# Kernel optimization log

Hardware: AMD Instinct MI355X
Metric: run time of the kernel (lower is better)

## Reference

```python
import jax, jax.numpy as jnp
import numpy as np

B, HW, FEAT = 64, 196, 2048
EMB, HID, ATT, VOCAB, T = 512, 1024, 512, 10000, 20
STEPS = T - 1  # pack_padded_sequence uses lengths - 1


def setup_inputs() -> dict:
    key = jax.random.key(0)
    ks = jax.random.split(key, 16)
    rn = lambda k, s, sc=0.02: jax.random.normal(k, s, jnp.float32) * sc
    return {
        "features": jax.random.normal(ks[0], (B, HW, FEAT), jnp.float32),
        "captions": jax.random.randint(ks[1], (B, T), 0, VOCAB),
        "lengths": jnp.full((B,), T, jnp.int32),  # uniform lengths -> constant batch per step
        "E": rn(ks[2], (VOCAB, EMB)),
        "W_feat": rn(ks[3], (EMB, FEAT)), "b_feat": jnp.zeros((EMB,), jnp.float32),
        "W1": rn(ks[4], (ATT, EMB)), "b1": jnp.zeros((ATT,), jnp.float32),
        "W2": rn(ks[5], (ATT, HID)), "b2": jnp.zeros((ATT,), jnp.float32),
        "V": rn(ks[6], (1, ATT)), "bV": jnp.zeros((1,), jnp.float32),
        "W_hi": rn(ks[7], (HID, EMB)), "b_hi": jnp.zeros((HID,), jnp.float32),
        "W_ci": rn(ks[8], (HID, EMB)), "b_ci": jnp.zeros((HID,), jnp.float32),
        "W_ih": rn(ks[9], (4 * HID, 2 * EMB)), "b_ih": jnp.zeros((4 * HID,), jnp.float32),
        "W_hh": rn(ks[10], (4 * HID, HID)), "b_hh": jnp.zeros((4 * HID,), jnp.float32),
        "W_out": rn(ks[11], (VOCAB, HID)), "b_out": jnp.zeros((VOCAB,), jnp.float32),
    }


def reference(features, captions, lengths, E, W_feat, b_feat, W1, b1, W2, b2,
              V, bV, W_hi, b_hi, W_ci, b_ci, W_ih, b_ih, W_hh, b_hh, W_out, b_out):
    # features -> embed space: [B, HW, EMB]
    f = jnp.einsum('bhc,ec->bhe', features, W_feat) + b_feat
    fmean = f.mean(axis=1)                      # [B, EMB]
    hx0 = fmean @ W_hi.T + b_hi                 # [B, HID]
    cx0 = fmean @ W_ci.T + b_ci                 # [B, HID]
    fa = jnp.einsum('bhe,ae->bha', f, W1) + b1  # W1(features), [B, HW, ATT]

    emb = E[captions]                           # [B, T, EMB]
    xs = jnp.swapaxes(emb[:, :STEPS], 0, 1)     # [STEPS, B, EMB] teacher-forced inputs

    def step(carry, x):
        hx, cx = carry
        # Bahdanau attention
        ha = hx @ W2.T + b2                             # [B, ATT]
        score = jnp.tanh(fa + ha[:, None, :])           # [B, HW, ATT]
        logits = jnp.einsum('bha,oa->bho', score, V) + bV   # [B, HW, 1]
        w = jax.nn.softmax(logits, axis=1)              # softmax over HW
        ctx = jnp.sum(w * f, axis=1)                    # [B, EMB]
        # LSTMCell (PyTorch gate order: i, f, g, o)
        inp = jnp.concatenate([x, ctx], axis=1)         # [B, 2*EMB]
        gates = inp @ W_ih.T + b_ih + hx @ W_hh.T + b_hh
        i_g, f_g, g_g, o_g = jnp.split(gates, 4, axis=1)
        cx_n = jax.nn.sigmoid(f_g) * cx + jax.nn.sigmoid(i_g) * jnp.tanh(g_g)
        hx_n = jax.nn.sigmoid(o_g) * jnp.tanh(cx_n)
        out = hx_n @ W_out.T + b_out                    # dropout = identity (eval)
        return (hx_n, cx_n), out

    _, outs = jax.lax.scan(step, (hx0, cx0), xs)        # [STEPS, B, VOCAB]
    # torch.cat(outputs) over constant per-step batch == flatten time-major
    return outs.reshape(STEPS * B, VOCAB)
```

## Files before the change

kernel.cpp:

```cpp
#include <hip/hip_runtime.h>
#include <hip/hip_bf16.h>
#include <math.h>

#define BB 64
#define HW 196
#define FEAT 2048
#define EMB 512
#define HID 1024
#define ATT 512
#define VOCAB 10000
#define TT 20
#define STEPS 19

using bfrag = __attribute__((ext_vector_type(8))) short;
using f32x4 = __attribute__((ext_vector_type(4))) float;

__device__ __forceinline__ float sigmoid_fast(float x) { return 1.0f / (1.0f + __expf(-x)); }
__device__ __forceinline__ float tanh_fast(float x) {
    float e = __expf(2.0f * x);
    return 1.0f - 2.0f / (e + 1.0f);
}
__device__ __forceinline__ ushort f2bf_rne(float f) {
    unsigned u = __float_as_uint(f);
    unsigned r = (u + 0x7FFFu + ((u >> 16) & 1u)) >> 16;
    return (ushort)r;
}
__device__ __forceinline__ float bf2f(ushort h) {
    return __uint_as_float(((unsigned)h) << 16);
}
__device__ __forceinline__ int sw_idx(int row, int g) { return row * 4 + (g ^ ((row >> 1) & 3)); }

__global__ __launch_bounds__(256) void k_split(const float* __restrict__ x,
                                               ushort* __restrict__ hi,
                                               ushort* __restrict__ lo, int n)
{
    int i4 = (blockIdx.x * 256 + threadIdx.x) * 4;
    if (i4 >= n) return;
    float4 v = *(const float4*)(x + i4);
    float av[4] = {v.x, v.y, v.z, v.w};
    #pragma unroll
    for (int j = 0; j < 4; ++j) {
        ushort h = f2bf_rne(av[j]);
        hi[i4 + j] = h;
        lo[i4 + j] = f2bf_rne(av[j] - bf2f(h));
    }
}

template<bool NFAST>
__global__ __launch_bounds__(256) void mfma_g(
    const float* __restrict__ A,
    const ushort* __restrict__ Bhi, const ushort* __restrict__ Blo,
    const float* __restrict__ bias, float* __restrict__ C,
    int N, int K, int Bld, int ldc, int NXB, int NMB)
{
    __shared__ __align__(16) ushort sAh[256 * 8];
    __shared__ __align__(16) ushort sAl[256 * 8];
    __shared__ __align__(16) ushort sBh[512 * 8];
    __shared__ __align__(16) ushort sBl[512 * 8];

    const int tid = threadIdx.x;

    const int nwg = NXB * NMB;
    const int q = nwg >> 3, r = nwg & 7;
    const int xcd = blockIdx.x & 7, sidx = blockIdx.x >> 3;
    const int wg = (xcd < r) ? (xcd * (q + 1) + sidx)
                             : (r * (q + 1) + (xcd - r) * q + sidx);
    int im, inb;
    if (NFAST) { inb = wg % NXB; im = wg / NXB; }
    else       { im = wg % NMB; inb = wg / NMB; }
    const int m0 = im * 64;
    const int n0 = inb * 128;

    const int lane = tid & 63;
    const int w = tid >> 6;
    const int mh = (w & 1) * 32;
    const int nh = (w >> 1) * 64;
    const int g = lane >> 4, l15 = lane & 15;

    f32x4 acc[2][4] = {};

    for (int k0 = 0; k0 < K; k0 += 32) {
        __syncthreads();
        {
            int r_ = tid >> 2, g_ = tid & 3;
            const float* ap = A + (size_t)(m0 + r_) * K + k0 + g_ * 8;
            float av[8];
            *(float4*)(av)     = *(const float4*)(ap);
            *(float4*)(av + 4) = *(const float4*)(ap + 4);
            bfrag vh, vl;
            #pragma unroll
            for (int j = 0; j < 8; ++j) {
                ushort h = f2bf_rne(av[j]);
                vh[j] = (short)h;
                vl[j] = (short)f2bf_rne(av[j] - bf2f(h));
            }
            int c = sw_idx(r_, g_) * 8;
            *(bfrag*)&sAh[c] = vh;
            *(bfrag*)&sAl[c] = vl;
        }
        #pragma unroll
        for (int i = 0; i < 4; ++i) {
            int c = tid + i * 256;
            int pl = c >> 9, idx2 = c & 511;
            int r_ = idx2 >> 2, g_ = idx2 & 3;
            int brow = min(n0 + r_, N - 1);
            const ushort* src = (pl ? Blo : Bhi) + (size_t)brow * Bld + k0 + g_ * 8;
            int cc = sw_idx(r_, g_) * 8;
            if (pl) *(bfrag*)&sBl[cc] = *(const bfrag*)src;
            else    *(bfrag*)&sBh[cc] = *(const bfrag*)src;
        }
        __syncthreads();

        bfrag ah[2], al[2], bh[4], bl[4];
        #pragma unroll
        for (int s = 0; s < 2; ++s) {
            int c = sw_idx(mh + s * 16 + l15, g) * 8;
            ah[s] = *(const bfrag*)&sAh[c];
            al[s] = *(const bfrag*)&sAl[c];
        }
        #pragma unroll
        for (int u = 0; u < 4; ++u) {
            int c = sw_idx(nh + u * 16 + l15, g) * 8;
            bh[u] = *(const bfrag*)&sBh[c];
            bl[u] = *(const bfrag*)&sBl[c];
        }
        #pragma unroll
        for (int s = 0; s < 2; ++s)
            #pragma unroll
            for (int u = 0; u < 4; ++u) {
                acc[s][u] = __builtin_amdgcn_mfma_f32_16x16x32_bf16(ah[s], bh[u], acc[s][u], 0, 0, 0);
                acc[s][u] = __builtin_amdgcn_mfma_f32_16x16x32_bf16(ah[s], bl[u], acc[s][u], 0, 0, 0);
                acc[s][u] = __builtin_amdgcn_mfma_f32_16x16x32_bf16(al[s], bh[u], acc[s][u], 0, 0, 0);
            }
    }

    #pragma unroll
    for (int s = 0; s < 2; ++s)
        #pragma unroll
        for (int u = 0; u < 4; ++u) {
            int col = n0 + nh + u * 16 + l15;
            if (col < N) {
                float bv = bias ? bias[col] : 0.f;
                #pragma unroll
                for (int rr = 0; rr < 4; ++rr) {
                    int row = m0 + mh + s * 16 + g * 4 + rr;
                    C[(size_t)row * ldc + col] = acc[s][u][rr] + bv;
                }
            }
        }
}

__global__ __launch_bounds__(256) void k_fmean2(const float* __restrict__ f,
                                                float* __restrict__ fmean)
{
    __shared__ float part[128];
    int blk = blockIdx.x;
    int b = blk >> 2, eq = blk & 3;
    int el = threadIdx.x & 127, half = threadIdx.x >> 7;
    int e = eq * 128 + el;
    const float* fb = f + (size_t)b * HW * EMB + e;
    float s = 0.f;
    int h0 = half * 98;
    for (int h = h0; h < h0 + 98; ++h) s += fb[(size_t)h * EMB];
    if (half) part[el] = s;
    __syncthreads();
    if (!half) fmean[b * EMB + e] = (s + part[el]) * (1.0f / HW);
}

__global__ __launch_bounds__(256) void k_init2(
    const float* __restrict__ fmean,
    const float* __restrict__ W_hi, const float* __restrict__ b_hi,
    const float* __restrict__ W_ci, const float* __restrict__ b_ci,
    float* __restrict__ hx, float* __restrict__ cx,
    ushort* __restrict__ hxp_h, ushort* __restrict__ hxp_l)
{
    int o = blockIdx.x * 256 + threadIdx.x;
    int b = o >> 11, uu = o & 2047;
    bool isC = uu >= 1024;
    int u = uu & 1023;
    const float4* wr = (const float4*)((isC ? W_ci : W_hi) + (size_t)u * EMB);
    const float4* fm = (const float4*)(fmean + (size_t)b * EMB);
    float s = isC ? b_ci[u] : b_hi[u];
    #pragma unroll 8
    for (int k = 0; k < EMB / 4; ++k) {
        float4 wv = wr[k], xv = fm[k];
        s += wv.x*xv.x + wv.y*xv.y + wv.z*xv.z + wv.w*xv.w;
    }
    int idx = b * HID + u;
    if (isC) cx[idx] = s;
    else {
        hx[idx] = s;
        ushort hh = f2bf_rne(s);
        hxp_h[idx] = hh;
        hxp_l[idx] = f2bf_rne(s - bf2f(hh));
    }
}

__global__ __launch_bounds__(128) void k_embed(const int* __restrict__ cap,
                                               const float* __restrict__ E,
                                               float* __restrict__ xs_f)
{
    int blk = blockIdx.x;
    int t = blk / BB, b = blk % BB;
    int c = cap[b * TT + t];
    const float4* src = (const float4*)(E + (size_t)c * EMB);
    float4* dst = (float4*)(xs_f + ((size_t)t * BB + b) * EMB);
    dst[threadIdx.x] = src[threadIdx.x];
}

__global__ __launch_bounds__(256) void k_ha(
    const float* __restrict__ hx, const float* __restrict__ W2,
    const float* __restrict__ b2, float* __restrict__ ha)
{
    __shared__ __align__(16) float hx_s[8][1028];
    __shared__ float part[256];
    const int tid = threadIdx.x;
    const int a0 = (blockIdx.x >> 3) * 16;
    const int b0 = (blockIdx.x & 7) * 8;

    for (int i = tid; i < 8 * 256; i += 256) {
        int r = i >> 8, c4 = i & 255;
        *(float4*)&hx_s[r][c4 * 4] = *(const float4*)(hx + (size_t)(b0 + r) * HID + c4 * 4);
    }
    __syncthreads();

    const int a_i = tid >> 4;
    const int b_i = (tid >> 1) & 7;
    const int half = tid & 1;
    const float4* wr = (const float4*)(W2 + (size_t)(a0 + a_i) * HID + half * 512);
    const float* xr = &hx_s[b_i][half * 512];
    float s = 0.f;
    #pragma unroll 8
    for (int i = 0; i < 128; ++i) {
        float4 w = wr[i];
        float4 x = *(const float4*)(xr + i * 4);
        s += w.x*x.x + w.y*x.y + w.z*x.z + w.w*x.w;
    }
    part[tid] = s;
    __syncthreads();
    if (!half)
        ha[(size_t)(b0 + b_i) * ATT + a0 + a_i] = part[tid] + part[tid + 1] + b2[a0 + a_i];
}

__global__ __launch_bounds__(1024) void k_att(
    const float* __restrict__ f, const float* __restrict__ fa,
    const float* __restrict__ ha, const float* __restrict__ V,
    ushort* __restrict__ ctx_hi, ushort* __restrict__ ctx_lo)
{
    __shared__ __align__(16) float smem[2048];
    const int b = blockIdx.x;
    const int tid = threadIdx.x;
    const int lane = tid & 63;
    const int wid = tid >> 6;

    float* ha_s = smem;
    float* V_s  = smem + 512;
    float* w_s  = smem + 1024;
    float* red  = smem + 1280;
    float* pc   = smem + 1536;

    if (tid < ATT) { ha_s[tid] = ha[b * ATT + tid]; V_s[tid] = V[tid]; }
    __syncthreads();

    for (int h = wid; h < HW; h += 16) {
        const float4* fr = (const float4*)(fa + ((size_t)b * HW + h) * ATT);
        float s = 0.f;
        #pragma unroll
        for (int q = 0; q < 2; ++q) {
            int i4 = q * 64 + lane;
            float4 fv = fr[i4];
            float4 hv = *(const float4*)&ha_s[i4 * 4];
            float4 vv = *(const float4*)&V_s[i4 * 4];
            s += tanh_fast(fv.x + hv.x) * vv.x + tanh_fast(fv.y + hv.y) * vv.y
               + tanh_fast(fv.z + hv.z) * vv.z + tanh_fast(fv.w + hv.w) * vv.w;
        }
        #pragma unroll
        for (int off = 32; off > 0; off >>= 1) s += __shfl_down(s, off);
        if (lane == 0) w_s[h] = s;
    }
    __syncthreads();

    float v = (tid < HW) ? w_s[tid] : -INFINITY;
    if (tid < 256) red[tid] = v;
    __syncthreads();
    for (int s2 = 128; s2 > 0; s2 >>= 1) {
        if (tid < s2) red[tid] = fmaxf(red[tid], red[tid + s2]);
        __syncthreads();
    }
    float mx = red[0];
    __syncthreads();
    float e = (tid < HW) ? __expf(v - mx) : 0.f;
    if (tid < 256) red[tid] = e;
    __syncthreads();
    for (int s2 = 128; s2 > 0; s2 >>= 1) {
        if (tid < s2) red[tid] += red[tid + s2];
        __syncthreads();
    }
    float inv = 1.0f / red[0];
    if (tid < HW) w_s[tid] = e * inv;
    __syncthreads();

    {
        int e0 = tid & 511, grp = tid >> 9;
        const float* fb = f + (size_t)b * HW * EMB + e0;
        float s = 0.f;
        int h0 = grp * 98;
        for (int h = h0; h < h0 + 98; ++h)
            s = fmaf(w_s[h], fb[(size_t)h * EMB], s);
        if (grp) pc[e0] = s;
        __syncthreads();
        if (!grp) {
            float c = s + pc[e0];
            ushort ch = f2bf_rne(c);
            ctx_hi[b * EMB + e0] = ch;
            ctx_lo[b * EMB + e0] = f2bf_rne(c - bf2f(ch));
        }
    }
}

__global__ __launch_bounds__(512) void k_gates_lstm(
    const float* __restrict__ gxs_t,
    const ushort* __restrict__ cth, const ushort* __restrict__ ctl,
    const ushort* __restrict__ hxh, const ushort* __restrict__ hxl,
    const ushort* __restrict__ wihh, const ushort* __restrict__ wihl,
    const ushort* __restrict__ whhh, const ushort* __restrict__ whhl,
    const float* __restrict__ b_ih, const float* __restrict__ b_hh,
    float* __restrict__ hx, float* __restrict__ cx,
    ushort* __restrict__ nxh, ushort* __restrict__ nxl,
    float* __restrict__ hx_all_t)
{
    __shared__ float sg[2][64][16];
    const int tid = threadIdx.x, bk = blockIdx.x;
    const int lane = tid & 63, wid = tid >> 6;
    const int mt = wid & 3, kh = wid >> 2;
    const int l15 = lane & 15, g = lane >> 4;
    const int arow = mt * 16 + l15;
    const int ncol = (l15 >> 2) * 1024 + bk * 4 + (l15 & 3);
    const int koff = g * 8;

    f32x4 acc0 = {}, acc1 = {};

    if (kh == 0) {
        {
            const ushort* ah = cth + (size_t)arow * 512 + koff;
            const ushort* al = ctl + (size_t)arow * 512 + koff;
            const ushort* bh = wihh + (size_t)ncol * 1024 + 512 + koff;
            const ushort* bl = wihl + (size_t)ncol * 1024 + 512 + koff;
            #pragma unroll 4
            for (int kk = 0; kk < 16; ++kk) {
                bfrag a_h = *(const bfrag*)(ah + kk * 32);
                bfrag a_l = *(const bfrag*)(al + kk * 32);
                bfrag b_h = *(const bfrag*)(bh + kk * 32);
                bfrag b_l = *(const bfrag*)(bl + kk * 32);
                acc0 = __builtin_amdgcn_mfma_f32_16x16x32_bf16(a_h, b_h, acc0, 0, 0, 0);
                acc1 = __builtin_amdgcn_mfma_f32_16x16x32_bf16(a_h, b_l, acc1, 0, 0, 0);
                acc1 = __builtin_amdgcn_mfma_f32_16x16x32_bf16(a_l, b_h, acc1, 0, 0, 0);
            }
        }
        {
            const ushort* ah = hxh + (size_t)arow * 1024 + koff;
            const ushort* al = hxl + (size_t)arow * 1024 + koff;
            const ushort* bh = whhh + (size_t)ncol * 1024 + koff;
            const ushort* bl = whhl + (size_t)ncol * 1024 + koff;
            #pragma unroll 4
            for (int kk = 0; kk < 8; ++kk) {
                bfrag a_h = *(const bfrag*)(ah + kk * 32);
                bfrag a_l = *(const bfrag*)(al + kk * 32);
                bfrag b_h = *(const bfrag*)(bh + kk * 32);
                bfrag b_l = *(const bfrag*)(bl + kk * 32);
                acc0 = __builtin_amdgcn_mfma_f32_16x16x32_bf16(a_h, b_h, acc0, 0, 0, 0);
                acc1 = __builtin_amdgcn_mfma_f32_16x16x32_bf16(a_h, b_l, acc1, 0, 0, 0);
                acc1 = __builtin_amdgcn_mfma_f32_16x16x32_bf16(a_l, b_h, acc1, 0, 0, 0);
            }
        }
    } else {
        const ushort* ah = hxh + (size_t)arow * 1024 + 256 + koff;
        const ushort* al = hxl + (size_t)arow * 1024 + 256 + koff;
        const ushort* bh = whhh + (size_t)ncol * 1024 + 256 + koff;
        const ushort* bl = whhl + (size_t)ncol * 1024 + 256 + koff;
        #pragma unroll 4
        for (int kk = 0; kk < 24; ++kk) {
            bfrag a_h = *(const bfrag*)(ah + kk * 32);
            bfrag a_l = *(const bfrag*)(al + kk * 32);
            bfrag b_h = *(const bfrag*)(bh + kk * 32);
            bfrag b_l = *(const bfrag*)(bl + kk * 32);
            acc0 = __builtin_amdgcn_mfma_f32_16x16x32_bf16(a_h, b_h, acc0, 0, 0, 0);
            acc1 = __builtin_amdgcn_mfma_f32_16x16x32_bf16(a_h, b_l, acc1, 0, 0, 0);
            acc1 = __builtin_amdgcn_mfma_f32_16x16x32_bf16(a_l, b_h, acc1, 0, 0, 0);
        }
    }

    #pragma unroll
    for (int rr = 0; rr < 4; ++rr)
        sg[kh][mt * 16 + g * 4 + rr][l15] = acc0[rr] + acc1[rr];
    __syncthreads();

    if (tid < 256) {
        int b = tid >> 2, uu = tid & 3;
        int u = bk * 4 + uu;
        const float* gx = gxs_t + (size_t)b * 4096;
        float gi = sg[0][b][uu]      + sg[1][b][uu]      + gx[u]        + b_ih[u]        + b_hh[u];
        float gf = sg[0][b][4 + uu]  + sg[1][b][4 + uu]  + gx[1024 + u] + b_ih[1024 + u] + b_hh[1024 + u];
        float gg = sg[0][b][8 + uu]  + sg[1][b][8 + uu]  + gx[2048 + u] + b_ih[2048 + u] + b_hh[2048 + u];
        float go = sg[0][b][12 + uu] + sg[1][b][12 + uu] + gx[3072 + u] + b_ih[3072 + u] + b_hh[3072 + u];
        int idx = b * 1024 + u;
        float c = sigmoid_fast(gf) * cx[idx] + sigmoid_fast(gi) * tanh_fast(gg);
        float h = sigmoid_fast(go) * tanh_fast(c);
        cx[idx] = c;
        hx[idx] = h;
        hx_all_t[idx] = h;
        ushort hh = f2bf_rne(h);
        nxh[idx] = hh;
        nxl[idx] = f2bf_rne(h - bf2f(hh));
    }
}

extern "C" void kernel_launch(void* const* d_in, const int* in_sizes, int n_in,
                              void* d_out, int out_size, void* d_ws, size_t ws_size,
                              hipStream_t stream) {
    const float* features = (const float*)d_in[0];
    const int*   captions = (const int*)d_in[1];
    const float* E      = (const float*)d_in[3];
    const float* W_feat = (const float*)d_in[4];
    const float* b_feat = (const float*)d_in[5];
    const float* W1     = (const float*)d_in[6];
    const float* b1     = (const float*)d_in[7];
    const float* W2     = (const float*)d_in[8];
    const float* b2     = (const float*)d_in[9];
    const float* V      = (const float*)d_in[10];
    const float* W_hi   = (const float*)d_in[12];
    const float* b_hi   = (const float*)d_in[13];
    const float* W_ci   = (const float*)d_in[14];
    const float* b_ci   = (const float*)d_in[15];
    const float* W_ih   = (const float*)d_in[16];
    const float* b_ih   = (const float*)d_in[17];
    const float* W_hh   = (const float*)d_in[18];
    const float* b_hh   = (const float*)d_in[19];
    const float* W_out  = (const float*)d_in[20];
    const float* b_out  = (const float*)d_in[21];
    float* out = (float*)d_out;

    float* ws = (float*)d_ws;
    float* f_buf   = ws;
    float* fa_buf  = f_buf + 6422528;
    float* fmean   = fa_buf + 6422528;
    float* hx      = fmean + 32768;
    float* cx      = hx + 65536;
    float* hx_all  = cx + 65536;
    float* ha      = hx_all + 1310720;
    float* xs_f    = ha + 32768;
    float* gxs     = xs_f + 622592;
    ushort* p = (ushort*)(gxs + 4980736);
    ushort* wfeat_hi = p;            p += 1048576;
    ushort* wfeat_lo = p;            p += 1048576;
    ushort* w1_hi    = p;            p += 262144;
    ushort* w1_lo    = p;            p += 262144;
    ushort* wih_hi   = p;            p += 4194304;
    ushort* wih_lo   = p;            p += 4194304;
    ushort* whh_hi   = p;            p += 4194304;
    ushort* whh_lo   = p;            p += 4194304;
    ushort* ctx_hi   = p;            p += 32768;
    ushort* ctx_lo   = p;            p += 32768;
    ushort* hxp      = p;            p += 262144;
    ushort* wout_hi = (ushort*)f_buf;
    ushort* wout_lo = wout_hi + 10240000;

    k_split<<<1048576 / 4 / 256, 256, 0, stream>>>(W_feat, wfeat_hi, wfeat_lo, 1048576);
    k_split<<<262144 / 4 / 256, 256, 0, stream>>>(W1, w1_hi, w1_lo, 262144);
    k_split<<<4194304 / 4 / 256, 256, 0, stream>>>(W_ih, wih_hi, wih_lo, 4194304);
    k_split<<<4194304 / 4 / 256, 256, 0, stream>>>(W_hh, whh_hi, whh_lo, 4194304);
    k_embed<<<STEPS * BB, 128, 0, stream>>>(captions, E, xs_f);
    mfma_g<true><<<784, 256, 0, stream>>>(
        features, wfeat_hi, wfeat_lo, b_feat, f_buf, 512, 2048, 2048, 512, 4, 196);
    mfma_g<true><<<784, 256, 0, stream>>>(
        f_buf, w1_hi, w1_lo, b1, fa_buf, 512, 512, 512, 512, 4, 196);
    mfma_g<false><<<608, 256, 0, stream>>>(
        xs_f, wih_hi, wih_lo, nullptr, gxs, 4096, 512, 1024, 4096, 32, 19);
    k_fmean2<<<256, 256, 0, stream>>>(f_buf, fmean);
    k_init2<<<512, 256, 0, stream>>>(fmean, W_hi, b_hi, W_ci, b_ci,
                                     hx, cx, hxp, hxp + 65536);

    for (int t = 0; t < STEPS; ++t) {
        ushort* hx_rd = hxp + (size_t)(t & 1) * 131072;
        ushort* hx_wr = hxp + (size_t)((t + 1) & 1) * 131072;
        k_ha<<<256, 256, 0, stream>>>(hx, W2, b2, ha);
        k_att<<<BB, 1024, 0, stream>>>(f_buf, fa_buf, ha, V, ctx_hi, ctx_lo);
        k_gates_lstm<<<256, 512, 0, stream>>>(
            gxs + (size_t)t * BB * 4096,
            ctx_hi, ctx_lo, hx_rd, hx_rd + 65536,
            wih_hi, wih_lo, whh_hi, whh_lo, b_ih, b_hh,
            hx, cx, hx_wr, hx_wr + 65536,
            hx_all + (size_t)t * BB * HID);
    }

    k_split<<<10240000 / 4 / 256, 256, 0, stream>>>(W_out, wout_hi, wout_lo, 10240000);
    mfma_g<false><<<1501, 256, 0, stream>>>(
        hx_all, wout_hi, wout_lo, b_out, out, VOCAB, HID, 1024, VOCAB, 79, 19);
}
```

Measured before the change: 1.573 ms.

## Store attention projection in bf16 and use direct global-to-LDS loads for B

The W1 projection output (fa) is now written as bf16 instead of fp32, which halves the bytes the per-step attention kernel reads from it on each of the 19 steps. The attention kernel keeps ha and V in registers instead of shared memory. The GEMM's B-tile staging now uses global_load_lds direct-to-LDS loads with addresses precomputed outside the k-loop. The workspace layout is reshuffled to make room for the bf16 buffer. Rounding fa to bf16 adds precision loss inside the tanh attention scores.

Result: slower. 1.983 ms (+26.1%).

```diff
diff --git a/kernel.cpp b/kernel.cpp
--- a/kernel.cpp
+++ b/kernel.cpp
@@ -46,11 +46,12 @@
     }
 }
 
-template<bool NFAST>
+template<bool NFAST, bool BF16OUT>
 __global__ __launch_bounds__(256) void mfma_g(
     const float* __restrict__ A,
     const ushort* __restrict__ Bhi, const ushort* __restrict__ Blo,
     const float* __restrict__ bias, float* __restrict__ C,
+    ushort* __restrict__ C16,
     int N, int K, int Bld, int ldc, int NXB, int NMB)
 {
     __shared__ __align__(16) ushort sAh[256 * 8];
@@ -77,16 +78,33 @@
     const int nh = (w >> 1) * 64;
     const int g = lane >> 4, l15 = lane & 15;
 
+    const int rA = tid >> 2, gA = tid & 3;
+    const float* apA = A + (size_t)(m0 + rA) * K + gA * 8;
+    const int cA = sw_idx(rA, gA) * 8;
+
+    const ushort* bsrc[4];
+    ushort* bdst[4];
+    #pragma unroll
+    for (int i = 0; i < 4; ++i) {
+        int cbase = i * 256 + w * 64;
+        int plane = cbase >> 9;
+        int ccb = cbase & 511;
+        int cc = ccb + lane;
+        int row = cc >> 2;
+        int g_ = (cc & 3) ^ ((row >> 1) & 3);
+        int brow = min(n0 + row, N - 1);
+        bsrc[i] = (plane ? Blo : Bhi) + (size_t)brow * Bld + g_ * 8;
+        bdst[i] = (plane ? sBl : sBh) + ccb * 8;
+    }
+
     f32x4 acc[2][4] = {};
 
     for (int k0 = 0; k0 < K; k0 += 32) {
         __syncthreads();
         {
-            int r_ = tid >> 2, g_ = tid & 3;
-            const float* ap = A + (size_t)(m0 + r_) * K + k0 + g_ * 8;
             float av[8];
-            *(float4*)(av)     = *(const float4*)(ap);
-            *(float4*)(av + 4) = *(const float4*)(ap + 4);
+            *(float4*)(av)     = *(const float4*)(apA + k0);
+            *(float4*)(av + 4) = *(const float4*)(apA + k0 + 4);
             bfrag vh, vl;
             #pragma unroll
             for (int j = 0; j < 8; ++j) {
@@ -94,21 +112,14 @@
                 vh[j] = (short)h;
                 vl[j] = (short)f2bf_rne(av[j] - bf2f(h));
             }
-            int c = sw_idx(r_, g_) * 8;
-            *(bfrag*)&sAh[c] = vh;
-            *(bfrag*)&sAl[c] = vl;
-        }
-        #pragma unroll
-        for (int i = 0; i < 4; ++i) {
-            int c = tid + i * 256;
-            int pl = c >> 9, idx2 = c & 511;
-            int r_ = idx2 >> 2, g_ = idx2 & 3;
-            int brow = min(n0 + r_, N - 1);
-            const ushort* src = (pl ? Blo : Bhi) + (size_t)brow * Bld + k0 + g_ * 8;
-            int cc = sw_idx(r_, g_) * 8;
-            if (pl) *(bfrag*)&sBl[cc] = *(const bfrag*)src;
-            else    *(bfrag*)&sBh[cc] = *(const bfrag*)src;
-        }
+            *(bfrag*)&sAh[cA] = vh;
+            *(bfrag*)&sAl[cA] = vl;
+        }
+        #pragma unroll
+        for (int i = 0; i < 4; ++i)
+            __builtin_amdgcn_global_load_lds(
+                (const __attribute__((address_space(1))) void*)(bsrc[i] + k0),
+                (__attribute__((address_space(3))) void*)bdst[i], 16, 0, 0);
         __syncthreads();
 
         bfrag ah[2], al[2], bh[4], bl[4];
@@ -144,7 +155,9 @@
                 #pragma unroll
                 for (int rr = 0; rr < 4; ++rr) {
                     int row = m0 + mh + s * 16 + g * 4 + rr;
-                    C[(size_t)row * ldc + col] = acc[s][u][rr] + bv;
+                    float v = acc[s][u][rr] + bv;
+                    if (BF16OUT) C16[(size_t)row * ldc + col] = f2bf_rne(v);
+                    else         C[(size_t)row * ldc + col] = v;
                 }
             }
         }
@@ -243,37 +256,34 @@
 }
 
 __global__ __launch_bounds__(1024) void k_att(
-    const float* __restrict__ f, const float* __restrict__ fa,
+    const float* __restrict__ f, const ushort* __restrict__ fa16,
     const float* __restrict__ ha, const float* __restrict__ V,
     ushort* __restrict__ ctx_hi, ushort* __restrict__ ctx_lo)
 {
-    __shared__ __align__(16) float smem[2048];
+    __shared__ __align__(16) float smem[1024];
     const int b = blockIdx.x;
     const int tid = threadIdx.x;
     const int lane = tid & 63;
     const int wid = tid >> 6;
 
-    float* ha_s = smem;
-    float* V_s  = smem + 512;
-    float* w_s  = smem + 1024;
-    float* red  = smem + 1280;
-    float* pc   = smem + 1536;
-
-    if (tid < ATT) { ha_s[tid] = ha[b * ATT + tid]; V_s[tid] = V[tid]; }
-    __syncthreads();
+    float* w_s = smem;
+    float* red = smem + 256;
+    float* pc  = smem + 512;
+
+    float hr[8], vr[8];
+    {
+        const float4* hp = (const float4*)(ha + (size_t)b * ATT + lane * 8);
+        const float4* vp = (const float4*)(V + lane * 8);
+        *(float4*)(hr) = hp[0]; *(float4*)(hr + 4) = hp[1];
+        *(float4*)(vr) = vp[0]; *(float4*)(vr + 4) = vp[1];
+    }
 
     for (int h = wid; h < HW; h += 16) {
-        const float4* fr = (const float4*)(fa + ((size_t)b * HW + h) * ATT);
+        bfrag fv = *(const bfrag*)(fa16 + ((size_t)b * HW + h) * ATT + lane * 8);
         float s = 0.f;
         #pragma unroll
-        for (int q = 0; q < 2; ++q) {
-            int i4 = q * 64 + lane;
-            float4 fv = fr[i4];
-            float4 hv = *(const float4*)&ha_s[i4 * 4];
-            float4 vv = *(const float4*)&V_s[i4 * 4];
-            s += tanh_fast(fv.x + hv.x) * vv.x + tanh_fast(fv.y + hv.y) * vv.y
-               + tanh_fast(fv.z + hv.z) * vv.z + tanh_fast(fv.w + hv.w) * vv.w;
-        }
+        for (int j = 0; j < 8; ++j)
+            s += tanh_fast(bf2f((ushort)fv[j]) + hr[j]) * vr[j];
         #pragma unroll
         for (int off = 32; off > 0; off >>= 1) s += __shfl_down(s, off);
         if (lane == 0) w_s[h] = s;
@@ -442,15 +452,14 @@
 
     float* ws = (float*)d_ws;
     float* f_buf   = ws;
-    float* fa_buf  = f_buf + 6422528;
-    float* fmean   = fa_buf + 6422528;
+    float* gxs     = f_buf + 6422528;
+    float* xs_f    = gxs + 4980736;
+    float* fmean   = xs_f + 622592;
     float* hx      = fmean + 32768;
     float* cx      = hx + 65536;
     float* hx_all  = cx + 65536;
     float* ha      = hx_all + 1310720;
-    float* xs_f    = ha + 32768;
-    float* gxs     = xs_f + 622592;
-    ushort* p = (ushort*)(gxs + 4980736);
+    ushort* p = (ushort*)(ha + 32768);
     ushort* wfeat_hi = p;            p += 1048576;
     ushort* wfeat_lo = p;            p += 1048576;
     ushort* w1_hi    = p;            p += 262144;
@@ -462,6 +471,7 @@
     ushort* ctx_hi   = p;            p += 32768;
     ushort* ctx_lo   = p;            p += 32768;
     ushort* hxp      = p;            p += 262144;
+    ushort* fa16     = p;            p += 6422528;
     ushort* wout_hi = (ushort*)f_buf;
     ushort* wout_lo = wout_hi + 10240000;
 
@@ -470,12 +480,15 @@
     k_split<<<4194304 / 4 / 256, 256, 0, stream>>>(W_ih, wih_hi, wih_lo, 4194304);
     k_split<<<4194304 / 4 / 256, 256, 0, stream>>>(W_hh, whh_hi, whh_lo, 4194304);
     k_embed<<<STEPS * BB, 128, 0, stream>>>(captions, E, xs_f);
-    mfma_g<true><<<784, 256, 0, stream>>>(
-        features, wfeat_hi, wfeat_lo, b_feat, f_buf, 512, 2048, 2048, 512, 4, 196);
-    mfma_g<true><<<784, 256, 0, stream>>>(
-        f_buf, w1_hi, w1_lo, b1, fa_buf, 512, 512, 512, 512, 4, 196);
-    mfma_g<false><<<608, 256, 0, stream>>>(
-        xs_f, wih_hi, wih_lo, nullptr, gxs, 4096, 512, 1024, 4096, 32, 19);
+    mfma_g<true, false><<<784, 256, 0, stream>>>(
+        features, wfeat_hi, wfeat_lo, b_feat, f_buf, nullptr,
+        512, 2048, 2048, 512, 4, 196);
+    mfma_g<true, true><<<784, 256, 0, stream>>>(
+        f_buf, w1_hi, w1_lo, b1, nullptr, fa16,
+        512, 512, 512, 512, 4, 196);
+    mfma_g<false, false><<<608, 256, 0, stream>>>(
+        xs_f, wih_hi, wih_lo, nullptr, gxs, nullptr,
+        4096, 512, 1024, 4096, 32, 19);
     k_fmean2<<<256, 256, 0, stream>>>(f_buf, fmean);
     k_init2<<<512, 256, 0, stream>>>(fmean, W_hi, b_hi, W_ci, b_ci,
                                      hx, cx, hxp, hxp + 65536);
@@ -484,7 +497,7 @@
         ushort* hx_rd = hxp + (size_t)(t & 1) * 131072;
         ushort* hx_wr = hxp + (size_t)((t + 1) & 1) * 131072;
         k_ha<<<256, 256, 0, stream>>>(hx, W2, b2, ha);
-        k_att<<<BB, 1024, 0, stream>>>(f_buf, fa_buf, ha, V, ctx_hi, ctx_lo);
+        k_att<<<BB, 1024, 0, stream>>>(f_buf, fa16, ha, V, ctx_hi, ctx_lo);
         k_gates_lstm<<<256, 512, 0, stream>>>(
             gxs + (size_t)t * BB * 4096,
             ctx_hi, ctx_lo, hx_rd, hx_rd + 65536,
@@ -494,6 +507,7 @@
     }
 
     k_split<<<10240000 / 4 / 256, 256, 0, stream>>>(W_out, wout_hi, wout_lo, 10240000);
-    mfma_g<false><<<1501, 256, 0, stream>>>(
-        hx_all, wout_hi, wout_lo, b_out, out, VOCAB, HID, 1024, VOCAB, 79, 19);
-}
+    mfma_g<false, false><<<1501, 256, 0, stream>>>(
+        hx_all, wout_hi, wout_lo, b_out, out, nullptr,
+        VOCAB, HID, 1024, VOCAB, 79, 19);
+}
```
